# Kernel tuning notes

Hardware: AMD Instinct MI355X
Metric: run time of the kernel (lower is better)

## Reference

```python
import jax, jax.numpy as jnp
import numpy as np


def setup_inputs() -> dict:
    key = jax.random.key(0)
    k1, k2, k3, k4, k5 = jax.random.split(key, 5)
    return {
        "d1": jax.random.normal(k1, (2, 4096, 512), dtype=jnp.float32),
        "d2": jax.random.normal(k2, (2, 512, 4096), dtype=jnp.float32),
        "d3": jax.random.normal(k3, (2, 4096, 512), dtype=jnp.float32),
        "d4": jax.random.normal(k4, (512, 512), dtype=jnp.float32),
        "d5": jax.random.normal(k5, (1, 512), dtype=jnp.float32),
    }


def reference(d1, d2, d3, d4, d5):
    # attention core: scores = d1 @ d2 -> [2, 4096, 4096]
    scores = jnp.einsum('bsd,bdt->bst', d1, d2)
    attn = jax.nn.softmax(scores, axis=2)
    # weighted values: [2, 4096, 512]
    ctx = jnp.einsum('bst,btd->bsd', attn, d3)
    # flatten batch*seq and apply final projection with bias (addmm)
    x = ctx.reshape(8192, 512)
    return d5 + x @ d4  # d5 [1,512] broadcasts over rows
```

## Files before the change

kernel.cpp:

```cpp
#include <hip/hip_runtime.h>

typedef unsigned short u16;
typedef __attribute__((ext_vector_type(8))) short short8;
typedef __attribute__((ext_vector_type(4))) float f32x4;

#define MFMA16(a, b, c) __builtin_amdgcn_mfma_f32_16x16x32_bf16((a), (b), (c), 0, 0, 0)

constexpr int Bb = 2, Ss = 4096, Tt = 4096, Dd = 512;
constexpr int BM = 64, BN = 64, TP = 4;
constexpr int TPART = Tt / TP;
constexpr int TCH = TPART / BN;

constexpr size_t SZ_BF = (size_t)Bb * Ss * Dd * 2;
constexpr size_t O_QH  = 0;
constexpr size_t O_QL  = O_QH + SZ_BF;
constexpr size_t O_D2TH = O_QL + SZ_BF;
constexpr size_t O_D2TL = O_D2TH + SZ_BF;
constexpr size_t O_D3T  = O_D2TL + SZ_BF;
constexpr size_t O_D4T  = O_D3T + SZ_BF;
constexpr size_t O_CTX  = O_D4T + (size_t)512 * 512 * 2;
constexpr size_t O_OP   = O_CTX + SZ_BF;
constexpr size_t O_MP   = O_OP + (size_t)TP * SZ_BF;
constexpr size_t O_LP   = O_MP + (size_t)TP * Bb * Ss * 4;

__device__ __forceinline__ u16 f2bf(float x) {
  union { float f; unsigned u; } v; v.f = x;
  unsigned r = v.u + 0x7fffu + ((v.u >> 16) & 1u);
  return (u16)(r >> 16);
}
__device__ __forceinline__ float bf2f(u16 h) {
  union { unsigned u; float f; } v; v.u = ((unsigned)h) << 16;
  return v.f;
}

__global__ void cvt_split_kernel(const float* __restrict__ in,
                                 u16* __restrict__ outh, u16* __restrict__ outl) {
  const int i = blockIdx.x * 256 + threadIdx.x;
  float4 v = ((const float4*)in)[i];
  ushort4 hh, ll;
  hh.x = f2bf(v.x); ll.x = f2bf(v.x - bf2f(hh.x));
  hh.y = f2bf(v.y); ll.y = f2bf(v.y - bf2f(hh.y));
  hh.z = f2bf(v.z); ll.z = f2bf(v.z - bf2f(hh.z));
  hh.w = f2bf(v.w); ll.w = f2bf(v.w - bf2f(hh.w));
  ((ushort4*)outh)[i] = hh;
  ((ushort4*)outl)[i] = ll;
}

__global__ void transpose_split_kernel(const float* __restrict__ in,
                                       u16* __restrict__ outh,
                                       u16* __restrict__ outl,
                                       int R, int C) {
  __shared__ float tile[32][33];
  int b = blockIdx.z;
  const float* inb = in + (size_t)b * R * C;
  int x = blockIdx.x * 32 + threadIdx.x;
  int y0 = blockIdx.y * 32;
  for (int j = threadIdx.y; j < 32; j += 8)
    tile[j][threadIdx.x] = inb[(size_t)(y0 + j) * C + x];
  __syncthreads();
  size_t ob = (size_t)b * C * R;
  for (int j = threadIdx.y; j < 32; j += 8) {
    float v = tile[threadIdx.x][j];
    size_t oi = ob + (size_t)(blockIdx.x * 32 + j) * R + (y0 + threadIdx.x);
    u16 h = f2bf(v);
    outh[oi] = h;
    if (outl) outl[oi] = f2bf(v - bf2f(h));
  }
}

__global__ __launch_bounds__(256, 2)
void flash_part_kernel(const u16* __restrict__ qh_g,
                       const u16* __restrict__ ql_g,
                       const u16* __restrict__ d2th,
                       const u16* __restrict__ d2tl,
                       const u16* __restrict__ d3t,
                       u16* __restrict__ opart,
                       float* __restrict__ mpart,
                       float* __restrict__ lpart) {
  __shared__ u16 kh[64 * 136], kl[64 * 136];
  __shared__ u16 vb[128 * 72];
  __shared__ u16 ph[64 * 72];

  const int tid = threadIdx.x;
  const int wave = tid >> 6, lane = tid & 63, quad = lane >> 4, l15 = lane & 15;
  const int m0 = wave * 16;
  const int s0 = blockIdx.x * BM, tp = blockIdx.y, b = blockIdx.z;

  f32x4 o_acc[32];
#pragma unroll
  for (int i = 0; i < 32; i++) o_acc[i] = (f32x4){0.f, 0.f, 0.f, 0.f};
  float m_r[4] = {-INFINITY, -INFINITY, -INFINITY, -INFINITY};
  float l_r[4] = {0.f, 0.f, 0.f, 0.f};

  const u16* qh_row = qh_g + ((size_t)b * Ss + s0 + m0 + l15) * Dd + quad * 8;
  const u16* ql_row = ql_g + ((size_t)b * Ss + s0 + m0 + l15) * Dd + quad * 8;
  const u16* kh_b = d2th + (size_t)b * Tt * Dd;
  const u16* kl_b = d2tl + (size_t)b * Tt * Dd;
  const u16* v_b  = d3t  + (size_t)b * Dd * Tt;

  const int krow = tid >> 2, kcol = (tid & 3) * 32;
  const int vrow = tid >> 1, vcol = (tid & 1) * 32;

  for (int tc = 0; tc < TCH; tc++) {
    const int t0 = tp * TPART + tc * BN;
    f32x4 s_acc[4];
#pragma unroll
    for (int nt = 0; nt < 4; nt++) s_acc[nt] = (f32x4){0.f, 0.f, 0.f, 0.f};

    for (int ds = 0; ds < 4; ds++) {
      const int d0 = ds * 128;
      __syncthreads();
      {
        const u16* sh = kh_b + (size_t)(t0 + krow) * Dd + d0 + kcol;
        const u16* sl = kl_b + (size_t)(t0 + krow) * Dd + d0 + kcol;
        u16* dh = &kh[krow * 136 + kcol];
        u16* dl = &kl[krow * 136 + kcol];
#pragma unroll
        for (int u = 0; u < 32; u += 8) {
          *(uint4*)(dh + u) = *(const uint4*)(sh + u);
          *(uint4*)(dl + u) = *(const uint4*)(sl + u);
        }
      }
      __syncthreads();
      short8 ah[4], al[4];
#pragma unroll
      for (int ks = 0; ks < 4; ks++) {
        ah[ks] = *(const short8*)(qh_row + d0 + ks * 32);
        al[ks] = *(const short8*)(ql_row + d0 + ks * 32);
      }
#pragma unroll
      for (int ks = 0; ks < 4; ks++) {
        const int kk = ks * 32 + quad * 8;
#pragma unroll
        for (int nt = 0; nt < 4; nt++) {
          short8 bh = *(const short8*)&kh[(nt * 16 + l15) * 136 + kk];
          short8 bl = *(const short8*)&kl[(nt * 16 + l15) * 136 + kk];
          s_acc[nt] = MFMA16(ah[ks], bh, s_acc[nt]);
          s_acc[nt] = MFMA16(al[ks], bh, s_acc[nt]);
          s_acc[nt] = MFMA16(ah[ks], bl, s_acc[nt]);
        }
      }
    }

    float alpha[4], psum[4];
#pragma unroll
    for (int r = 0; r < 4; r++) {
      float v = fmaxf(fmaxf(s_acc[0][r], s_acc[1][r]), fmaxf(s_acc[2][r], s_acc[3][r]));
      v = fmaxf(v, __shfl_xor(v, 1));
      v = fmaxf(v, __shfl_xor(v, 2));
      v = fmaxf(v, __shfl_xor(v, 4));
      v = fmaxf(v, __shfl_xor(v, 8));
      float mn = fmaxf(m_r[r], v);
      alpha[r] = __expf(m_r[r] - mn);
      m_r[r] = mn;
      psum[r] = 0.f;
    }
#pragma unroll
    for (int nt = 0; nt < 4; nt++) {
#pragma unroll
      for (int r = 0; r < 4; r++) {
        float p = __expf(s_acc[nt][r] - m_r[r]);
        psum[r] += p;
        ph[(m0 + quad * 4 + r) * 72 + nt * 16 + l15] = f2bf(p);
      }
    }
#pragma unroll
    for (int r = 0; r < 4; r++) {
      float v = psum[r];
      v += __shfl_xor(v, 1);
      v += __shfl_xor(v, 2);
      v += __shfl_xor(v, 4);
      v += __shfl_xor(v, 8);
      l_r[r] = l_r[r] * alpha[r] + v;
    }
#pragma unroll
    for (int j = 0; j < 32; j++) {
#pragma unroll
      for (int r = 0; r < 4; r++) o_acc[j][r] *= alpha[r];
    }

#pragma unroll
    for (int nc = 0; nc < 4; nc++) {
      __syncthreads();
      {
        const u16* sv = v_b + (size_t)(nc * 128 + vrow) * Tt + t0 + vcol;
        u16* dv = &vb[vrow * 72 + vcol];
#pragma unroll
        for (int u = 0; u < 32; u += 8) *(uint4*)(dv + u) = *(const uint4*)(sv + u);
      }
      __syncthreads();
#pragma unroll
      for (int ks = 0; ks < 2; ks++) {
        const int kk = ks * 32 + quad * 8;
        short8 ap = *(const short8*)&ph[(m0 + l15) * 72 + kk];
#pragma unroll
        for (int nt = 0; nt < 8; nt++) {
          short8 bv = *(const short8*)&vb[(nt * 16 + l15) * 72 + kk];
          o_acc[nc * 8 + nt] = MFMA16(ap, bv, o_acc[nc * 8 + nt]);
        }
      }
    }
  }

  const size_t obase = (((size_t)tp * Bb + b) * Ss + s0) * Dd;
#pragma unroll
  for (int j = 0; j < 32; j++) {
    const int col = (j >> 3) * 128 + (j & 7) * 16 + l15;
#pragma unroll
    for (int r = 0; r < 4; r++) {
      const int row = m0 + quad * 4 + r;
      opart[obase + (size_t)row * Dd + col] = f2bf(o_acc[j][r]);
    }
  }
  if (l15 == 0) {
    const size_t sbase = ((size_t)tp * Bb + b) * Ss + s0;
#pragma unroll
    for (int r = 0; r < 4; r++) {
      const int row = m0 + quad * 4 + r;
      mpart[sbase + row] = m_r[r];
      lpart[sbase + row] = l_r[r];
    }
  }
}

__global__ void combine_kernel(const u16* __restrict__ opart,
                               const float* __restrict__ mpart,
                               const float* __restrict__ lpart,
                               u16* __restrict__ ctx) {
  const int idx = blockIdx.x * blockDim.x + threadIdx.x;
  const int vpr = Dd / 8;
  const int row = idx / vpr;
  const int dv = (idx % vpr) * 8;
  float mv[TP], mM = -INFINITY;
#pragma unroll
  for (int p = 0; p < TP; p++) {
    mv[p] = mpart[(size_t)p * Bb * Ss + row];
    mM = fmaxf(mM, mv[p]);
  }
  float w[TP], denom = 0.f;
#pragma unroll
  for (int p = 0; p < TP; p++) {
    float e = __expf(mv[p] - mM);
    w[p] = e;
    denom += e * lpart[(size_t)p * Bb * Ss + row];
  }
  const float inv = 1.0f / denom;
  float acc[8];
#pragma unroll
  for (int e = 0; e < 8; e++) acc[e] = 0.f;
#pragma unroll
  for (int p = 0; p < TP; p++) {
    uint4 raw = *(const uint4*)&opart[(size_t)p * Bb * Ss * Dd + (size_t)row * Dd + dv];
    const u16* u = (const u16*)&raw;
#pragma unroll
    for (int e = 0; e < 8; e++) acc[e] += w[p] * bf2f(u[e]);
  }
  u16 outv[8];
#pragma unroll
  for (int e = 0; e < 8; e++) outv[e] = f2bf(acc[e] * inv);
  *(uint4*)&ctx[(size_t)row * Dd + dv] = *(const uint4*)outv;
}

__global__ __launch_bounds__(256, 2)
void proj_kernel(const u16* __restrict__ ctx,
                 const u16* __restrict__ d4t,
                 const float* __restrict__ d5,
                 float* __restrict__ out) {
  __shared__ u16 a_lds[128 * 40], b_lds[128 * 40];
  const int tid = threadIdx.x;
  const int wave = tid >> 6, lane = tid & 63, quad = lane >> 4, l15 = lane & 15;
  const int m0w = (wave & 1) * 64, n0w = (wave >> 1) * 64;
  const int bm = blockIdx.x, bn = blockIdx.y;
  f32x4 acc[4][4];
#pragma unroll
  for (int i = 0; i < 4; i++)
#pragma unroll
    for (int j = 0; j < 4; j++) acc[i][j] = (f32x4){0.f, 0.f, 0.f, 0.f};

  const int srow = tid >> 2, scol = (tid & 3) * 8;
  for (int kt = 0; kt < 16; kt++) {
    const int k0 = kt * 32;
    __syncthreads();
#pragma unroll
    for (int pass = 0; pass < 2; pass++) {
      const int row = srow + pass * 64;
      *(uint4*)&a_lds[row * 40 + scol] =
          *(const uint4*)&ctx[(size_t)(bm * 128 + row) * Dd + k0 + scol];
      *(uint4*)&b_lds[row * 40 + scol] =
          *(const uint4*)&d4t[(size_t)(bn * 128 + row) * Dd + k0 + scol];
    }
    __syncthreads();
    short8 af[4], bfr[4];
#pragma unroll
    for (int i = 0; i < 4; i++)
      af[i] = *(const short8*)&a_lds[(m0w + 16 * i + l15) * 40 + quad * 8];
#pragma unroll
    for (int j = 0; j < 4; j++)
      bfr[j] = *(const short8*)&b_lds[(n0w + 16 * j + l15) * 40 + quad * 8];
#pragma unroll
    for (int i = 0; i < 4; i++)
#pragma unroll
      for (int j = 0; j < 4; j++) acc[i][j] = MFMA16(af[i], bfr[j], acc[i][j]);
  }
#pragma unroll
  for (int j = 0; j < 4; j++) {
    const int colg = bn * 128 + n0w + 16 * j + l15;
    const float bias = d5[colg];
#pragma unroll
    for (int i = 0; i < 4; i++) {
#pragma unroll
      for (int r = 0; r < 4; r++) {
        const int rowg = bm * 128 + m0w + 16 * i + quad * 4 + r;
        out[(size_t)rowg * 512 + colg] = acc[i][j][r] + bias;
      }
    }
  }
}

extern "C" void kernel_launch(void* const* d_in, const int* in_sizes, int n_in,
                              void* d_out, int out_size, void* d_ws, size_t ws_size,
                              hipStream_t stream) {
  (void)in_sizes; (void)n_in; (void)out_size; (void)ws_size;
  const float* d1 = (const float*)d_in[0];
  const float* d2 = (const float*)d_in[1];
  const float* d3 = (const float*)d_in[2];
  const float* d4 = (const float*)d_in[3];
  const float* d5 = (const float*)d_in[4];
  float* out = (float*)d_out;
  char* ws = (char*)d_ws;

  u16* qh_g = (u16*)(ws + O_QH);
  u16* ql_g = (u16*)(ws + O_QL);
  u16* d2th = (u16*)(ws + O_D2TH);
  u16* d2tl = (u16*)(ws + O_D2TL);
  u16* d3t  = (u16*)(ws + O_D3T);
  u16* d4t  = (u16*)(ws + O_D4T);
  u16* ctx  = (u16*)(ws + O_CTX);
  u16* opart = (u16*)(ws + O_OP);
  float* mpart = (float*)(ws + O_MP);
  float* lpart = (float*)(ws + O_LP);

  cvt_split_kernel<<<(Bb * Ss * Dd / 4) / 256, 256, 0, stream>>>(d1, qh_g, ql_g);
  transpose_split_kernel<<<dim3(128, 16, 2), dim3(32, 8), 0, stream>>>(d2, d2th, d2tl, 512, 4096);
  transpose_split_kernel<<<dim3(16, 128, 2), dim3(32, 8), 0, stream>>>(d3, d3t, nullptr, 4096, 512);
  transpose_split_kernel<<<dim3(16, 16, 1), dim3(32, 8), 0, stream>>>(d4, d4t, nullptr, 512, 512);

  flash_part_kernel<<<dim3(Ss / BM, TP, Bb), 256, 0, stream>>>(qh_g, ql_g, d2th, d2tl, d3t,
                                                               opart, mpart, lpart);
  combine_kernel<<<(Bb * Ss * Dd / 8) / 256, 256, 0, stream>>>(opart, mpart, lpart, ctx);
  proj_kernel<<<dim3(64, 4), 256, 0, stream>>>(ctx, d4t, d5, out);
}
```

Baseline: 516.9 us.

## Prefetch next K/V tiles into registers to overlap global loads with MFMA

```diff
diff --git a/kernel.cpp b/kernel.cpp
--- a/kernel.cpp
+++ b/kernel.cpp
@@ -101,33 +101,60 @@
   const int krow = tid >> 2, kcol = (tid & 3) * 32;
   const int vrow = tid >> 1, vcol = (tid & 1) * 32;
 
+  uint4 krg_h[4], krg_l[4], vrg[4];
+
+  auto loadK = [&](int t0, int d0) {
+    const u16* sh = kh_b + (size_t)(t0 + krow) * Dd + d0 + kcol;
+    const u16* sl = kl_b + (size_t)(t0 + krow) * Dd + d0 + kcol;
+#pragma unroll
+    for (int u = 0; u < 4; u++) {
+      krg_h[u] = *(const uint4*)(sh + u * 8);
+      krg_l[u] = *(const uint4*)(sl + u * 8);
+    }
+  };
+  auto writeK = [&]() {
+    u16* dh = &kh[krow * 136 + kcol];
+    u16* dl = &kl[krow * 136 + kcol];
+#pragma unroll
+    for (int u = 0; u < 4; u++) {
+      *(uint4*)(dh + u * 8) = krg_h[u];
+      *(uint4*)(dl + u * 8) = krg_l[u];
+    }
+  };
+  auto loadV = [&](int t0, int nc) {
+    const u16* sv = v_b + (size_t)(nc * 128 + vrow) * Tt + t0 + vcol;
+#pragma unroll
+    for (int u = 0; u < 4; u++) vrg[u] = *(const uint4*)(sv + u * 8);
+  };
+  auto writeV = [&]() {
+    u16* dv = &vb[vrow * 72 + vcol];
+#pragma unroll
+    for (int u = 0; u < 4; u++) *(uint4*)(dv + u * 8) = vrg[u];
+  };
+
+  loadK(tp * TPART, 0);
+
   for (int tc = 0; tc < TCH; tc++) {
     const int t0 = tp * TPART + tc * BN;
     f32x4 s_acc[4];
 #pragma unroll
     for (int nt = 0; nt < 4; nt++) s_acc[nt] = (f32x4){0.f, 0.f, 0.f, 0.f};
 
+#pragma unroll
     for (int ds = 0; ds < 4; ds++) {
       const int d0 = ds * 128;
       __syncthreads();
-      {
-        const u16* sh = kh_b + (size_t)(t0 + krow) * Dd + d0 + kcol;
-        const u16* sl = kl_b + (size_t)(t0 + krow) * Dd + d0 + kcol;
-        u16* dh = &kh[krow * 136 + kcol];
-        u16* dl = &kl[krow * 136 + kcol];
-#pragma unroll
-        for (int u = 0; u < 32; u += 8) {
-          *(uint4*)(dh + u) = *(const uint4*)(sh + u);
-          *(uint4*)(dl + u) = *(const uint4*)(sl + u);
-        }
-      }
-      __syncthreads();
+      writeK();
+      if (ds < 3) loadK(t0, d0 + 128);
+      else        loadV(t0, 0);
       short8 ah[4], al[4];
 #pragma unroll
       for (int ks = 0; ks < 4; ks++) {
         ah[ks] = *(const short8*)(qh_row + d0 + ks * 32);
         al[ks] = *(const short8*)(ql_row + d0 + ks * 32);
       }
+      __syncthreads();
+      __builtin_amdgcn_s_setprio(1);
 #pragma unroll
       for (int ks = 0; ks < 4; ks++) {
         const int kk = ks * 32 + quad * 8;
@@ -140,6 +167,7 @@
           s_acc[nt] = MFMA16(ah[ks], bl, s_acc[nt]);
         }
       }
+      __builtin_amdgcn_s_setprio(0);
     }
 
     float alpha[4], psum[4];
@@ -182,13 +210,14 @@
 #pragma unroll
     for (int nc = 0; nc < 4; nc++) {
       __syncthreads();
-      {
-        const u16* sv = v_b + (size_t)(nc * 128 + vrow) * Tt + t0 + vcol;
-        u16* dv = &vb[vrow * 72 + vcol];
-#pragma unroll
-        for (int u = 0; u < 32; u += 8) *(uint4*)(dv + u) = *(const uint4*)(sv + u);
+      writeV();
+      if (nc < 3) loadV(t0, nc + 1);
+      else {
+        const int tcn = (tc + 1 < TCH) ? (tc + 1) : 0;
+        loadK(tp * TPART + tcn * BN, 0);
       }
       __syncthreads();
+      __builtin_amdgcn_s_setprio(1);
 #pragma unroll
       for (int ks = 0; ks < 2; ks++) {
         const int kk = ks * 32 + quad * 8;
@@ -199,6 +228,7 @@
           o_acc[nc * 8 + nt] = MFMA16(ap, bv, o_acc[nc * 8 + nt]);
         }
       }
+      __builtin_amdgcn_s_setprio(0);
     }
   }
 
```

New measurement: 769.8 us. 1.49x slower.

## Double-buffer K/V tiles via direct global-to-LDS loads with XOR swizzle

Applied to the files above, without the earlier changes.

```diff
diff --git a/kernel.cpp b/kernel.cpp
--- a/kernel.cpp
+++ b/kernel.cpp
@@ -31,6 +31,11 @@
 __device__ __forceinline__ float bf2f(u16 h) {
   union { unsigned u; float f; } v; v.u = ((unsigned)h) << 16;
   return v.f;
+}
+
+__device__ __forceinline__ void gl_lds16(const u16* g, u16* l) {
+  __builtin_amdgcn_global_load_lds((const __attribute__((address_space(1))) void*)g,
+                                   (__attribute__((address_space(3))) void*)l, 16, 0, 0);
 }
 
 __global__ void cvt_split_kernel(const float* __restrict__ in,
@@ -68,7 +73,7 @@
   }
 }
 
-__global__ __launch_bounds__(256, 2)
+__global__ __launch_bounds__(256, 3)
 void flash_part_kernel(const u16* __restrict__ qh_g,
                        const u16* __restrict__ ql_g,
                        const u16* __restrict__ d2th,
@@ -77,14 +82,15 @@
                        u16* __restrict__ opart,
                        float* __restrict__ mpart,
                        float* __restrict__ lpart) {
-  __shared__ u16 kh[64 * 136], kl[64 * 136];
-  __shared__ u16 vb[128 * 72];
-  __shared__ u16 ph[64 * 72];
+  __shared__ __align__(1024) u16 sbuf[2][8192];
+  __shared__ __align__(16) u16 ph[64 * 72];
 
   const int tid = threadIdx.x;
   const int wave = tid >> 6, lane = tid & 63, quad = lane >> 4, l15 = lane & 15;
   const int m0 = wave * 16;
   const int s0 = blockIdx.x * BM, tp = blockIdx.y, b = blockIdx.z;
+  const int rr = lane >> 3, sl = lane & 7;
+  const int x7 = l15 & 7;
 
   f32x4 o_acc[32];
 #pragma unroll
@@ -98,8 +104,35 @@
   const u16* kl_b = d2tl + (size_t)b * Tt * Dd;
   const u16* v_b  = d3t  + (size_t)b * Dd * Tt;
 
-  const int krow = tid >> 2, kcol = (tid & 3) * 32;
-  const int vrow = tid >> 1, vcol = (tid & 1) * 32;
+  short8 qh_r[16], ql_r[16];
+#pragma unroll
+  for (int t = 0; t < 16; t++) {
+    qh_r[t] = *(const short8*)(qh_row + t * 32);
+    ql_r[t] = *(const short8*)(ql_row + t * 32);
+  }
+
+  auto issueK = [&](int t0, int d0, int bp) {
+#pragma unroll
+    for (int i = 0; i < 2; i++) {
+      const int r0 = wave * 16 + i * 8;
+      const int r = r0 + rr;
+      const size_t so = (size_t)(t0 + r) * Dd + d0 + ((sl ^ rr) << 3);
+      gl_lds16(kh_b + so, &sbuf[bp][r0 * 64]);
+      gl_lds16(kl_b + so, &sbuf[bp][4096 + r0 * 64]);
+    }
+  };
+  auto issueV = [&](int t0, int nc, int bp) {
+#pragma unroll
+    for (int i = 0; i < 4; i++) {
+      const int r0 = wave * 32 + i * 8;
+      const int r = r0 + rr;
+      gl_lds16(v_b + (size_t)(nc * 128 + r) * Tt + t0 + ((sl ^ rr) << 3),
+               &sbuf[bp][r0 * 64]);
+    }
+  };
+
+  issueK(tp * TPART, 0, 0);
+  __syncthreads();
 
   for (int tc = 0; tc < TCH; tc++) {
     const int t0 = tp * TPART + tc * BN;
@@ -107,39 +140,27 @@
 #pragma unroll
     for (int nt = 0; nt < 4; nt++) s_acc[nt] = (f32x4){0.f, 0.f, 0.f, 0.f};
 
-    for (int ds = 0; ds < 4; ds++) {
-      const int d0 = ds * 128;
+#pragma unroll
+    for (int u = 0; u < 8; u++) {
+      if (u < 7) issueK(t0, (u + 1) * 64, (u + 1) & 1);
+      else       issueV(t0, 0, (u + 1) & 1);
+      __builtin_amdgcn_s_setprio(1);
+#pragma unroll
+      for (int ks = 0; ks < 2; ks++) {
+        const int t = u * 2 + ks;
+        const int g = ks * 4 + quad;
+#pragma unroll
+        for (int nt = 0; nt < 4; nt++) {
+          const int off = (nt * 16 + l15) * 64 + ((g ^ x7) << 3);
+          short8 bh = *(const short8*)&sbuf[u & 1][off];
+          short8 bl = *(const short8*)&sbuf[u & 1][4096 + off];
+          s_acc[nt] = MFMA16(qh_r[t], bh, s_acc[nt]);
+          s_acc[nt] = MFMA16(ql_r[t], bh, s_acc[nt]);
+          s_acc[nt] = MFMA16(qh_r[t], bl, s_acc[nt]);
+        }
+      }
+      __builtin_amdgcn_s_setprio(0);
       __syncthreads();
-      {
-        const u16* sh = kh_b + (size_t)(t0 + krow) * Dd + d0 + kcol;
-        const u16* sl = kl_b + (size_t)(t0 + krow) * Dd + d0 + kcol;
-        u16* dh = &kh[krow * 136 + kcol];
-        u16* dl = &kl[krow * 136 + kcol];
-#pragma unroll
-        for (int u = 0; u < 32; u += 8) {
-          *(uint4*)(dh + u) = *(const uint4*)(sh + u);
-          *(uint4*)(dl + u) = *(const uint4*)(sl + u);
-        }
-      }
-      __syncthreads();
-      short8 ah[4], al[4];
-#pragma unroll
-      for (int ks = 0; ks < 4; ks++) {
-        ah[ks] = *(const short8*)(qh_row + d0 + ks * 32);
-        al[ks] = *(const short8*)(ql_row + d0 + ks * 32);
-      }
-#pragma unroll
-      for (int ks = 0; ks < 4; ks++) {
-        const int kk = ks * 32 + quad * 8;
-#pragma unroll
-        for (int nt = 0; nt < 4; nt++) {
-          short8 bh = *(const short8*)&kh[(nt * 16 + l15) * 136 + kk];
-          short8 bl = *(const short8*)&kl[(nt * 16 + l15) * 136 + kk];
-          s_acc[nt] = MFMA16(ah[ks], bh, s_acc[nt]);
-          s_acc[nt] = MFMA16(al[ks], bh, s_acc[nt]);
-          s_acc[nt] = MFMA16(ah[ks], bl, s_acc[nt]);
-        }
-      }
     }
 
     float alpha[4], psum[4];
@@ -181,24 +202,27 @@
 
 #pragma unroll
     for (int nc = 0; nc < 4; nc++) {
-      __syncthreads();
-      {
-        const u16* sv = v_b + (size_t)(nc * 128 + vrow) * Tt + t0 + vcol;
-        u16* dv = &vb[vrow * 72 + vcol];
-#pragma unroll
-        for (int u = 0; u < 32; u += 8) *(uint4*)(dv + u) = *(const uint4*)(sv + u);
-      }
-      __syncthreads();
+      const int u = 8 + nc;
+      if (nc < 3) issueV(t0, nc + 1, (u + 1) & 1);
+      else {
+        const int tcn = (tc + 1 < TCH) ? tc + 1 : 0;
+        issueK(tp * TPART + tcn * BN, 0, (u + 1) & 1);
+      }
+      __builtin_amdgcn_s_setprio(1);
 #pragma unroll
       for (int ks = 0; ks < 2; ks++) {
         const int kk = ks * 32 + quad * 8;
+        const int g = ks * 4 + quad;
         short8 ap = *(const short8*)&ph[(m0 + l15) * 72 + kk];
 #pragma unroll
         for (int nt = 0; nt < 8; nt++) {
-          short8 bv = *(const short8*)&vb[(nt * 16 + l15) * 72 + kk];
+          const int off = (nt * 16 + l15) * 64 + ((g ^ x7) << 3);
+          short8 bv = *(const short8*)&sbuf[u & 1][off];
           o_acc[nc * 8 + nt] = MFMA16(ap, bv, o_acc[nc * 8 + nt]);
         }
       }
+      __builtin_amdgcn_s_setprio(0);
+      __syncthreads();
     }
   }
 
```

Result: slower. 626.2 us (+21.1%).

## Double-buffer K/V tiles via direct global-to-LDS loads with XOR swizzle

Applied to the files above, without the earlier changes.

```diff
diff --git a/kernel.cpp b/kernel.cpp
--- a/kernel.cpp
+++ b/kernel.cpp
@@ -31,6 +31,11 @@
 __device__ __forceinline__ float bf2f(u16 h) {
   union { unsigned u; float f; } v; v.u = ((unsigned)h) << 16;
   return v.f;
+}
+
+__device__ __forceinline__ void gl_lds16(const u16* g, u16* l) {
+  __builtin_amdgcn_global_load_lds((const __attribute__((address_space(1))) void*)g,
+                                   (__attribute__((address_space(3))) void*)l, 16, 0, 0);
 }
 
 __global__ void cvt_split_kernel(const float* __restrict__ in,
@@ -77,14 +82,17 @@
                        u16* __restrict__ opart,
                        float* __restrict__ mpart,
                        float* __restrict__ lpart) {
-  __shared__ u16 kh[64 * 136], kl[64 * 136];
-  __shared__ u16 vb[128 * 72];
-  __shared__ u16 ph[64 * 72];
+  __shared__ __align__(1024) u16 sbuf[2][16384];
+  __shared__ __align__(16) u16 ph[64 * 72];
 
   const int tid = threadIdx.x;
   const int wave = tid >> 6, lane = tid & 63, quad = lane >> 4, l15 = lane & 15;
   const int m0 = wave * 16;
-  const int s0 = blockIdx.x * BM, tp = blockIdx.y, b = blockIdx.z;
+  const int wg = blockIdx.x;
+  const int xcd = wg & 7, sblk = wg >> 3;
+  const int tp = xcd >> 1, b = xcd & 1;
+  const int s0 = sblk * BM;
+  const int x7 = l15 & 7;
 
   f32x4 o_acc[32];
 #pragma unroll
@@ -98,48 +106,66 @@
   const u16* kl_b = d2tl + (size_t)b * Tt * Dd;
   const u16* v_b  = d3t  + (size_t)b * Dd * Tt;
 
-  const int krow = tid >> 2, kcol = (tid & 3) * 32;
-  const int vrow = tid >> 1, vcol = (tid & 1) * 32;
+  const int kr4 = lane >> 4, ks16 = lane & 15;
+  auto issueK = [&](int t0_, int d0_, int bp) {
+#pragma unroll
+    for (int i = 0; i < 4; i++) {
+      const int r0 = wave * 16 + i * 4;
+      const int r = r0 + kr4;
+      const size_t so = (size_t)(t0_ + r) * Dd + d0_ + ((ks16 ^ (r & 7)) << 3);
+      gl_lds16(kh_b + so, &sbuf[bp][r0 * 128]);
+      gl_lds16(kl_b + so, &sbuf[bp][8192 + r0 * 128]);
+    }
+  };
+  const int vr8 = lane >> 3, vs8 = lane & 7;
+  auto issueV = [&](int t0_, int vh, int bp) {
+#pragma unroll
+    for (int i = 0; i < 8; i++) {
+      const int r0 = wave * 64 + i * 8;
+      const int r = r0 + vr8;
+      gl_lds16(v_b + (size_t)(vh * 256 + r) * Tt + t0_ + ((vs8 ^ (r & 7)) << 3),
+               &sbuf[bp][r0 * 64]);
+    }
+  };
+
+  const int t00 = tp * TPART;
+  issueK(t00, 0, 0);
+  __syncthreads();
 
   for (int tc = 0; tc < TCH; tc++) {
-    const int t0 = tp * TPART + tc * BN;
+    const int t0 = t00 + tc * BN;
     f32x4 s_acc[4];
 #pragma unroll
     for (int nt = 0; nt < 4; nt++) s_acc[nt] = (f32x4){0.f, 0.f, 0.f, 0.f};
 
+#pragma unroll
     for (int ds = 0; ds < 4; ds++) {
+      const int p = ds & 1;
+      if (ds < 3) issueK(t0, (ds + 1) * 128, p ^ 1);
+      else        issueV(t0, 0, p ^ 1);
       const int d0 = ds * 128;
-      __syncthreads();
-      {
-        const u16* sh = kh_b + (size_t)(t0 + krow) * Dd + d0 + kcol;
-        const u16* sl = kl_b + (size_t)(t0 + krow) * Dd + d0 + kcol;
-        u16* dh = &kh[krow * 136 + kcol];
-        u16* dl = &kl[krow * 136 + kcol];
-#pragma unroll
-        for (int u = 0; u < 32; u += 8) {
-          *(uint4*)(dh + u) = *(const uint4*)(sh + u);
-          *(uint4*)(dl + u) = *(const uint4*)(sl + u);
-        }
-      }
-      __syncthreads();
       short8 ah[4], al[4];
 #pragma unroll
       for (int ks = 0; ks < 4; ks++) {
         ah[ks] = *(const short8*)(qh_row + d0 + ks * 32);
         al[ks] = *(const short8*)(ql_row + d0 + ks * 32);
       }
+      __builtin_amdgcn_s_setprio(1);
 #pragma unroll
       for (int ks = 0; ks < 4; ks++) {
-        const int kk = ks * 32 + quad * 8;
+        const int go = ((ks * 4 + quad) ^ x7) << 3;
 #pragma unroll
         for (int nt = 0; nt < 4; nt++) {
-          short8 bh = *(const short8*)&kh[(nt * 16 + l15) * 136 + kk];
-          short8 bl = *(const short8*)&kl[(nt * 16 + l15) * 136 + kk];
+          const int off = (nt * 16 + l15) * 128 + go;
+          short8 bh = *(const short8*)&sbuf[p][off];
+          short8 bl = *(const short8*)&sbuf[p][8192 + off];
           s_acc[nt] = MFMA16(ah[ks], bh, s_acc[nt]);
           s_acc[nt] = MFMA16(al[ks], bh, s_acc[nt]);
           s_acc[nt] = MFMA16(ah[ks], bl, s_acc[nt]);
         }
       }
+      __builtin_amdgcn_s_setprio(0);
+      __syncthreads();
     }
 
     float alpha[4], psum[4];
@@ -180,25 +206,28 @@
     }
 
 #pragma unroll
-    for (int nc = 0; nc < 4; nc++) {
-      __syncthreads();
-      {
-        const u16* sv = v_b + (size_t)(nc * 128 + vrow) * Tt + t0 + vcol;
-        u16* dv = &vb[vrow * 72 + vcol];
-#pragma unroll
-        for (int u = 0; u < 32; u += 8) *(uint4*)(dv + u) = *(const uint4*)(sv + u);
-      }
-      __syncthreads();
+    for (int vh = 0; vh < 2; vh++) {
+      const int p = vh;
+      if (vh == 0) issueV(t0, 1, 1);
+      else {
+        const int tcn = (tc + 1 < TCH) ? tc + 1 : 0;
+        issueK(t00 + tcn * BN, 0, 0);
+      }
+      __builtin_amdgcn_s_setprio(1);
 #pragma unroll
       for (int ks = 0; ks < 2; ks++) {
         const int kk = ks * 32 + quad * 8;
+        const int go = ((ks * 4 + quad) ^ x7) << 3;
         short8 ap = *(const short8*)&ph[(m0 + l15) * 72 + kk];
 #pragma unroll
-        for (int nt = 0; nt < 8; nt++) {
-          short8 bv = *(const short8*)&vb[(nt * 16 + l15) * 72 + kk];
-          o_acc[nc * 8 + nt] = MFMA16(ap, bv, o_acc[nc * 8 + nt]);
+        for (int ntl = 0; ntl < 16; ntl++) {
+          const int off = (ntl * 16 + l15) * 64 + go;
+          short8 bv = *(const short8*)&sbuf[p][off];
+          o_acc[vh * 16 + ntl] = MFMA16(ap, bv, o_acc[vh * 16 + ntl]);
         }
       }
+      __builtin_amdgcn_s_setprio(0);
+      __syncthreads();
     }
   }
 
@@ -345,8 +374,8 @@
   transpose_split_kernel<<<dim3(16, 128, 2), dim3(32, 8), 0, stream>>>(d3, d3t, nullptr, 4096, 512);
   transpose_split_kernel<<<dim3(16, 16, 1), dim3(32, 8), 0, stream>>>(d4, d4t, nullptr, 512, 512);
 
-  flash_part_kernel<<<dim3(Ss / BM, TP, Bb), 256, 0, stream>>>(qh_g, ql_g, d2th, d2tl, d3t,
-                                                               opart, mpart, lpart);
+  flash_part_kernel<<<dim3((Ss / BM) * TP * Bb), 256, 0, stream>>>(qh_g, ql_g, d2th, d2tl, d3t,
+                                                                   opart, mpart, lpart);
   combine_kernel<<<(Bb * Ss * Dd / 8) / 256, 256, 0, stream>>>(opart, mpart, lpart, ctx);
   proj_kernel<<<dim3(64, 4), 256, 0, stream>>>(ctx, d4t, d5, out);
 }
```

Result: slower. 620.0 us (+19.9%).
